# Kernel optimization log

Hardware: AMD Instinct MI355X
Metric: run time of the kernel (lower is better)

The kernel has to match this reference:

```python
import jax, jax.numpy as jnp
import numpy as np

EPS = 1e-12  # torch F.normalize eps

def _l2norm(v, axis):
    n = jnp.sqrt(jnp.sum(v * v, axis=axis, keepdims=True))
    return v / jnp.maximum(n, EPS)

def setup_inputs() -> dict:
    key = jax.random.key(0)
    k1, k2, k3 = jax.random.split(key, 3)
    N, C, H, W, K = 64, 512, 32, 32, 64
    x = jax.random.normal(k1, (N, C, H, W), dtype=jnp.float32)
    conv_w = jax.random.normal(k2, (K, C), dtype=jnp.float32) * 0.05
    centroids = jax.random.uniform(k3, (K, C), dtype=jnp.float32)
    return {"x": x, "conv_w": conv_w, "centroids": centroids}

def reference(x, conv_w, centroids):
    N, C, H, W = x.shape
    K = centroids.shape[0]
    # descriptor-wise L2 normalization over channel dim
    x = _l2norm(x, axis=1)
    xf = x.reshape(N, C, H * W)                       # (N, C, S)
    # 1x1 conv (no bias) == per-pixel matmul, then softmax over clusters
    logits = jnp.einsum('kc,ncs->nks', conv_w, xf)    # (N, K, S)
    a = jax.nn.softmax(logits, axis=1)                # softmax over clusters
    # vlad[n,k,:] = sum_s a[n,k,s] * (x[n,:,s] - centroid[k])
    # = (a @ x^T) - centroid * sum_s a   -- two GEMM-like ops, no (N,K,C,S) tensor
    vlad = jnp.einsum('nks,ncs->nkc', a, xf) - a.sum(axis=-1)[..., None] * centroids[None, :, :]
    # intra-normalization per cluster, flatten, global L2 norm
    vlad = _l2norm(vlad, axis=2)
    vlad = vlad.reshape(N, K * C)
    vlad = _l2norm(vlad, axis=1)
    return vlad
```

## Files before the change

kernel.cpp:

```cpp
#include <hip/hip_runtime.h>
#include <hip/hip_bf16.h>
#include <math.h>

#define EPSF 1e-12f

typedef __attribute__((ext_vector_type(8))) short bf16x8;
typedef __attribute__((ext_vector_type(4))) float f32x4;
typedef __attribute__((ext_vector_type(4))) short short4v;
typedef __attribute__((ext_vector_type(4))) unsigned short ushort4v;

static __device__ __forceinline__ short f2bf(float f) {
  union { __hip_bfloat16 h; short s; } u;
  u.h = __float2bfloat16(f);
  return u.s;
}

__global__ __launch_bounds__(256) void k2_mfma(
    const float* __restrict__ x, const float* __restrict__ w,
    unsigned short* __restrict__ ap, float* __restrict__ suma) {
  __shared__ __align__(16) float xf[64][70];
  __shared__ __align__(16) short wb[64][72];
  __shared__ __align__(16) float red[4][64];
  __shared__ float invs[64];
  __shared__ float gmaxs[64];
  __shared__ float gsums[64];

  const int n = blockIdx.y;
  const int s0 = blockIdx.x << 6;
  const int t = threadIdx.x;
  const int lane = t & 63;
  const int wid = t >> 6;
  const int col = t & 15;
  const int quad = (t >> 4) & 3;
  const int cr = t >> 4;
  const int sg = t & 15;

  f32x4 acc[4] = {{0,0,0,0},{0,0,0,0},{0,0,0,0},{0,0,0,0}};
  float ssq0 = 0.f, ssq1 = 0.f, ssq2 = 0.f, ssq3 = 0.f;

  for (int c0 = 0; c0 < 512; c0 += 64) {
#pragma unroll
    for (int p = 0; p < 4; ++p) {
      int c = cr + (p << 4);
      float4 g = *(const float4*)&x[((size_t)((n << 9) + c0 + c) << 10) + s0 + (sg << 2)];
      float2 glo; glo.x = g.x; glo.y = g.y;
      float2 ghi; ghi.x = g.z; ghi.y = g.w;
      *(float2*)&xf[c][sg << 2] = glo;
      *(float2*)&xf[c][(sg << 2) + 2] = ghi;
      ssq0 = fmaf(g.x, g.x, ssq0); ssq1 = fmaf(g.y, g.y, ssq1);
      ssq2 = fmaf(g.z, g.z, ssq2); ssq3 = fmaf(g.w, g.w, ssq3);
      float4 gw = *(const float4*)&w[(c << 9) + c0 + (sg << 2)];
      short4v hw; hw.x = f2bf(gw.x); hw.y = f2bf(gw.y); hw.z = f2bf(gw.z); hw.w = f2bf(gw.w);
      *(short4v*)&wb[c][sg << 2] = hw;
    }
    __syncthreads();
#pragma unroll
    for (int cc = 0; cc < 64; cc += 32) {
      bf16x8 af = *(const bf16x8*)&wb[(wid << 4) + col][cc + (quad << 3)];
      int cb = cc + (quad << 3);
#pragma unroll
      for (int sgr = 0; sgr < 4; ++sgr) {
        int sc = (sgr << 4) + col;
        bf16x8 bfr;
#pragma unroll
        for (int j = 0; j < 8; ++j) bfr[j] = f2bf(xf[cb + j][sc]);
        acc[sgr] = __builtin_amdgcn_mfma_f32_16x16x32_bf16(af, bfr, acc[sgr], 0, 0, 0);
      }
    }
    __syncthreads();
  }

  ssq0 += __shfl_xor(ssq0, 16, 64); ssq0 += __shfl_xor(ssq0, 32, 64);
  ssq1 += __shfl_xor(ssq1, 16, 64); ssq1 += __shfl_xor(ssq1, 32, 64);
  ssq2 += __shfl_xor(ssq2, 16, 64); ssq2 += __shfl_xor(ssq2, 32, 64);
  ssq3 += __shfl_xor(ssq3, 16, 64); ssq3 += __shfl_xor(ssq3, 32, 64);
  if (lane < 16) {
    float4 v; v.x = ssq0; v.y = ssq1; v.z = ssq2; v.w = ssq3;
    *(float4*)&red[wid][sg << 2] = v;
  }
  __syncthreads();
  if (t < 64) {
    float tot = red[0][t] + red[1][t] + red[2][t] + red[3][t];
    invs[t] = 1.0f / fmaxf(sqrtf(tot), EPSF);
  }
  __syncthreads();

  float li[4];
#pragma unroll
  for (int sgr = 0; sgr < 4; ++sgr) li[sgr] = invs[(sgr << 4) + col];
  float le[4][4];
#pragma unroll
  for (int sgr = 0; sgr < 4; ++sgr)
#pragma unroll
    for (int r = 0; r < 4; ++r) le[sgr][r] = acc[sgr][r] * li[sgr];

  float mx[4];
#pragma unroll
  for (int sgr = 0; sgr < 4; ++sgr) {
    float m = fmaxf(fmaxf(le[sgr][0], le[sgr][1]), fmaxf(le[sgr][2], le[sgr][3]));
    m = fmaxf(m, __shfl_xor(m, 16, 64));
    m = fmaxf(m, __shfl_xor(m, 32, 64));
    mx[sgr] = m;
  }
  if (lane < 16) {
#pragma unroll
    for (int sgr = 0; sgr < 4; ++sgr) red[wid][(sgr << 4) + sg] = mx[sgr];
  }
  __syncthreads();
  if (t < 64)
    gmaxs[t] = fmaxf(fmaxf(red[0][t], red[1][t]), fmaxf(red[2][t], red[3][t]));
  __syncthreads();

  float ps[4];
#pragma unroll
  for (int sgr = 0; sgr < 4; ++sgr) {
    float gm = gmaxs[(sgr << 4) + col];
    float p = 0.f;
#pragma unroll
    for (int r = 0; r < 4; ++r) {
      float e = __expf(le[sgr][r] - gm);
      le[sgr][r] = e;
      p += e;
    }
    p += __shfl_xor(p, 16, 64);
    p += __shfl_xor(p, 32, 64);
    ps[sgr] = p;
  }
  if (lane < 16) {
#pragma unroll
    for (int sgr = 0; sgr < 4; ++sgr) red[wid][(sgr << 4) + sg] = ps[sgr];
  }
  __syncthreads();
  if (t < 64) gsums[t] = red[0][t] + red[1][t] + red[2][t] + red[3][t];
  __syncthreads();

  float sk[4] = {0.f, 0.f, 0.f, 0.f};
#pragma unroll
  for (int sgr = 0; sgr < 4; ++sgr) {
    float rinv = 1.0f / gsums[(sgr << 4) + col];
#pragma unroll
    for (int r = 0; r < 4; ++r) {
      float av = le[sgr][r] * rinv;
      sk[r] += av;
      float apv = av * li[sgr];
      int k = (wid << 4) + (quad << 2) + r;
      ap[((size_t)((n << 6) + k) << 10) + s0 + (sgr << 4) + col] =
          (unsigned short)f2bf(apv);
    }
  }
#pragma unroll
  for (int r = 0; r < 4; ++r) {
    sk[r] += __shfl_xor(sk[r], 1, 64);
    sk[r] += __shfl_xor(sk[r], 2, 64);
    sk[r] += __shfl_xor(sk[r], 4, 64);
    sk[r] += __shfl_xor(sk[r], 8, 64);
  }
  if (col == 0) {
#pragma unroll
    for (int r = 0; r < 4; ++r)
      atomicAdd(&suma[(n << 6) + (wid << 4) + (quad << 2) + r], sk[r]);
  }
}

__global__ __launch_bounds__(256) void k3_mfma(
    const float* __restrict__ x, const unsigned short* __restrict__ ap,
    const float* __restrict__ cent, const float* __restrict__ suma,
    float* __restrict__ out, float* __restrict__ rnorm2) {
  __shared__ __align__(16) char sm[64 * 72 * 2 * 2];
  short (*xb)[72] = reinterpret_cast<short(*)[72]>(sm);
  short (*at)[72] = reinterpret_cast<short(*)[72]>(sm + 9216);
  float (*lt)[68] = reinterpret_cast<float(*)[68]>(sm);

  const int n = blockIdx.y;
  const int c0 = blockIdx.x << 6;
  const int t = threadIdx.x;
  const int lane = t & 63;
  const int wid = t >> 6;
  const int col = t & 15;
  const int quad = (t >> 4) & 3;
  const int cr = t >> 4;
  const int sg = t & 15;

  f32x4 acc[4] = {{0,0,0,0},{0,0,0,0},{0,0,0,0},{0,0,0,0}};

  for (int s0 = 0; s0 < 1024; s0 += 64) {
#pragma unroll
    for (int p = 0; p < 4; ++p) {
      int c = cr + (p << 4);
      float4 g = *(const float4*)&x[((size_t)((n << 9) + c0 + c) << 10) + s0 + (sg << 2)];
      short4v hx; hx.x = f2bf(g.x); hx.y = f2bf(g.y); hx.z = f2bf(g.z); hx.w = f2bf(g.w);
      *(short4v*)&xb[c][sg << 2] = hx;
      ushort4v a4 = *(const ushort4v*)&ap[((size_t)((n << 6) + c) << 10) + s0 + (sg << 2)];
      *(ushort4v*)&at[c][sg << 2] = a4;
    }
    __syncthreads();
#pragma unroll
    for (int ss = 0; ss < 64; ss += 32) {
      bf16x8 af = *(const bf16x8*)&xb[(wid << 4) + col][ss + (quad << 3)];
#pragma unroll
      for (int kt = 0; kt < 4; ++kt) {
        bf16x8 bfr = *(const bf16x8*)&at[(kt << 4) + col][ss + (quad << 3)];
        acc[kt] = __builtin_amdgcn_mfma_f32_16x16x32_bf16(af, bfr, acc[kt], 0, 0, 0);
      }
    }
    __syncthreads();
  }

  float sa[4];
#pragma unroll
  for (int kt = 0; kt < 4; ++kt) sa[kt] = suma[(n << 6) + (kt << 4) + col];
  const int crow = (wid << 4) + (quad << 2);
  float r2[4] = {0.f, 0.f, 0.f, 0.f};
#pragma unroll
  for (int kt = 0; kt < 4; ++kt) {
    int k = (kt << 4) + col;
#pragma unroll
    for (int r = 0; r < 4; ++r) {
      int c = crow + r;
      float ce = cent[(k << 9) + c0 + c];
      float val = acc[kt][r] - sa[kt] * ce;
      r2[kt] = fmaf(val, val, r2[kt]);
      lt[k][c] = val;
    }
  }
#pragma unroll
  for (int kt = 0; kt < 4; ++kt) {
    r2[kt] += __shfl_xor(r2[kt], 16, 64);
    r2[kt] += __shfl_xor(r2[kt], 32, 64);
  }
  if (lane < 16) {
#pragma unroll
    for (int kt = 0; kt < 4; ++kt)
      atomicAdd(&rnorm2[(n << 6) + (kt << 4) + sg], r2[kt]);
  }
  __syncthreads();
#pragma unroll
  for (int u = 0; u < 4; ++u) {
    int k = t >> 2;
    int c = ((t & 3) << 2) + (u << 4);
    float4 v = *(const float4*)&lt[k][c];
    *(float4*)&out[((size_t)((n << 6) + k) << 9) + c0 + c] = v;
  }
}

__global__ __launch_bounds__(64) void k4_factors(const float* __restrict__ rnorm2,
                                                 float* __restrict__ fac) {
  int n = blockIdx.x, k = threadIdx.x;
  float r2 = rnorm2[(n << 6) + k];
  float rn = sqrtf(r2);
  float f = 1.0f / fmaxf(rn, EPSF);
  float nr = rn * f;
  float g = nr * nr;
#pragma unroll
  for (int off = 32; off > 0; off >>= 1) g += __shfl_xor(g, off, 64);
  fac[(n << 6) + k] = f * (1.0f / fmaxf(sqrtf(g), EPSF));
}

__global__ __launch_bounds__(256) void k5_scale(const float* __restrict__ vlad,
                                                const float* __restrict__ fac,
                                                float* __restrict__ out) {
  int idx = blockIdx.x * 256 + threadIdx.x;
  float4 v = ((const float4*)vlad)[idx];
  float f = fac[idx >> 7];
  float4 o;
  o.x = v.x * f; o.y = v.y * f; o.z = v.z * f; o.w = v.w * f;
  ((float4*)out)[idx] = o;
}

extern "C" void kernel_launch(void* const* d_in, const int* in_sizes, int n_in,
                              void* d_out, int out_size, void* d_ws, size_t ws_size,
                              hipStream_t stream) {
  (void)in_sizes; (void)n_in; (void)out_size; (void)ws_size;
  const float* x = (const float*)d_in[0];
  const float* w = (const float*)d_in[1];
  const float* cent = (const float*)d_in[2];
  float* out = (float*)d_out;

  float* ws = (float*)d_ws;
  float* suma = ws;
  float* rnorm2 = ws + 4096;
  float* fac = ws + 8192;
  unsigned short* ap = (unsigned short*)(ws + 12288);

  hipMemsetAsync(ws, 0, 8192 * sizeof(float), stream);
  k2_mfma<<<dim3(16, 64), 256, 0, stream>>>(x, w, ap, suma);
  k3_mfma<<<dim3(8, 64), 256, 0, stream>>>(x, ap, cent, suma, out, rnorm2);
  k4_factors<<<64, 64, 0, stream>>>(rnorm2, fac);
  k5_scale<<<2048, 256, 0, stream>>>(out, fac, out);
}
```

Baseline: 259.0 us.

## Register-prefetch k3 tiles, swap grid order, fold factor kernel into scale

k3 now double-buffers its global loads in registers, issuing the next tile's x and assignment loads before the MFMAs on the current tile, so memory latency overlaps compute. The grid is transposed so consecutive blocks take different batch items instead of channel slices of the same item. The separate k4 factor kernel is removed: each k5 block recomputes the per-cluster and global norm factors from rnorm2, saving one launch at the cost of redundant sqrt work and extra register pressure.

```diff
diff --git a/kernel.cpp b/kernel.cpp
--- a/kernel.cpp
+++ b/kernel.cpp
@@ -162,6 +162,37 @@
   }
 }
 
+#define K3_LOADT(gx, ga, S0)                                                   \
+  do {                                                                         \
+    _Pragma("unroll") for (int p = 0; p < 4; ++p) {                            \
+      gx[p] = *(const float4*)(xbase + ((size_t)(p << 4) << 10) + (S0));       \
+      ga[p] = *(const ushort4v*)(abase + ((size_t)(p << 4) << 10) + (S0));     \
+    }                                                                          \
+  } while (0)
+
+#define K3_WRITET(gx, ga)                                                      \
+  do {                                                                         \
+    _Pragma("unroll") for (int p = 0; p < 4; ++p) {                            \
+      int c = cr + (p << 4);                                                   \
+      short4v hx;                                                              \
+      hx.x = f2bf(gx[p].x); hx.y = f2bf(gx[p].y);                              \
+      hx.z = f2bf(gx[p].z); hx.w = f2bf(gx[p].w);                              \
+      *(short4v*)&xb[c][sg << 2] = hx;                                         \
+      *(ushort4v*)&at[c][sg << 2] = ga[p];                                     \
+    }                                                                          \
+  } while (0)
+
+#define K3_MFMAT()                                                             \
+  do {                                                                         \
+    _Pragma("unroll") for (int ss = 0; ss < 64; ss += 32) {                    \
+      bf16x8 af = *(const bf16x8*)&xb[(wid << 4) + col][ss + (quad << 3)];     \
+      _Pragma("unroll") for (int kt = 0; kt < 4; ++kt) {                       \
+        bf16x8 bfr = *(const bf16x8*)&at[(kt << 4) + col][ss + (quad << 3)];   \
+        acc[kt] = __builtin_amdgcn_mfma_f32_16x16x32_bf16(af, bfr, acc[kt], 0, 0, 0); \
+      }                                                                        \
+    }                                                                          \
+  } while (0)
+
 __global__ __launch_bounds__(256) void k3_mfma(
     const float* __restrict__ x, const unsigned short* __restrict__ ap,
     const float* __restrict__ cent, const float* __restrict__ suma,
@@ -171,8 +202,8 @@
   short (*at)[72] = reinterpret_cast<short(*)[72]>(sm + 9216);
   float (*lt)[68] = reinterpret_cast<float(*)[68]>(sm);
 
-  const int n = blockIdx.y;
-  const int c0 = blockIdx.x << 6;
+  const int n = blockIdx.x;
+  const int c0 = blockIdx.y << 6;
   const int t = threadIdx.x;
   const int lane = t & 63;
   const int wid = t >> 6;
@@ -183,26 +214,26 @@
 
   f32x4 acc[4] = {{0,0,0,0},{0,0,0,0},{0,0,0,0},{0,0,0,0}};
 
-  for (int s0 = 0; s0 < 1024; s0 += 64) {
-#pragma unroll
-    for (int p = 0; p < 4; ++p) {
-      int c = cr + (p << 4);
-      float4 g = *(const float4*)&x[((size_t)((n << 9) + c0 + c) << 10) + s0 + (sg << 2)];
-      short4v hx; hx.x = f2bf(g.x); hx.y = f2bf(g.y); hx.z = f2bf(g.z); hx.w = f2bf(g.w);
-      *(short4v*)&xb[c][sg << 2] = hx;
-      ushort4v a4 = *(const ushort4v*)&ap[((size_t)((n << 6) + c) << 10) + s0 + (sg << 2)];
-      *(ushort4v*)&at[c][sg << 2] = a4;
-    }
-    __syncthreads();
-#pragma unroll
-    for (int ss = 0; ss < 64; ss += 32) {
-      bf16x8 af = *(const bf16x8*)&xb[(wid << 4) + col][ss + (quad << 3)];
-#pragma unroll
-      for (int kt = 0; kt < 4; ++kt) {
-        bf16x8 bfr = *(const bf16x8*)&at[(kt << 4) + col][ss + (quad << 3)];
-        acc[kt] = __builtin_amdgcn_mfma_f32_16x16x32_bf16(af, bfr, acc[kt], 0, 0, 0);
-      }
-    }
+  const float* xbase = &x[((size_t)((n << 9) + c0 + cr) << 10) + (sg << 2)];
+  const unsigned short* abase = &ap[((size_t)((n << 6) + cr) << 10) + (sg << 2)];
+
+  float4 gxA[4]; ushort4v gaA[4];
+  float4 gxB[4]; ushort4v gaB[4];
+
+  K3_LOADT(gxA, gaA, 0);
+#pragma unroll 1
+  for (int it = 0; it < 8; ++it) {
+    K3_WRITET(gxA, gaA);
+    __syncthreads();
+    K3_LOADT(gxB, gaB, (size_t)(((it << 1) + 1) << 6));
+    K3_MFMAT();
+    __syncthreads();
+    K3_WRITET(gxB, gaB);
+    __syncthreads();
+    if (it < 7) {
+      K3_LOADT(gxA, gaA, (size_t)(((it << 1) + 2) << 6));
+    }
+    K3_MFMAT();
     __syncthreads();
   }
 
@@ -243,25 +274,28 @@
   }
 }
 
-__global__ __launch_bounds__(64) void k4_factors(const float* __restrict__ rnorm2,
-                                                 float* __restrict__ fac) {
-  int n = blockIdx.x, k = threadIdx.x;
-  float r2 = rnorm2[(n << 6) + k];
-  float rn = sqrtf(r2);
-  float f = 1.0f / fmaxf(rn, EPSF);
-  float nr = rn * f;
-  float g = nr * nr;
-#pragma unroll
-  for (int off = 32; off > 0; off >>= 1) g += __shfl_xor(g, off, 64);
-  fac[(n << 6) + k] = f * (1.0f / fmaxf(sqrtf(g), EPSF));
-}
-
 __global__ __launch_bounds__(256) void k5_scale(const float* __restrict__ vlad,
-                                                const float* __restrict__ fac,
+                                                const float* __restrict__ rnorm2,
                                                 float* __restrict__ out) {
-  int idx = blockIdx.x * 256 + threadIdx.x;
+  __shared__ float gsh;
+  const int b = blockIdx.x;
+  const int t = threadIdx.x;
+  const int n = b >> 5;
+  if (t < 64) {
+    float rn = sqrtf(rnorm2[(n << 6) + t]);
+    float nr = rn / fmaxf(rn, EPSF);
+    float g = nr * nr;
+#pragma unroll
+    for (int off = 32; off > 0; off >>= 1) g += __shfl_xor(g, off, 64);
+    if (t == 0) gsh = g;
+  }
+  __syncthreads();
+  const float ginv = 1.0f / fmaxf(sqrtf(gsh), EPSF);
+  const int idx = (b << 8) + t;
+  const int kg = idx >> 7;
+  float rn = sqrtf(rnorm2[kg]);
+  float f = (1.0f / fmaxf(rn, EPSF)) * ginv;
   float4 v = ((const float4*)vlad)[idx];
-  float f = fac[idx >> 7];
   float4 o;
   o.x = v.x * f; o.y = v.y * f; o.z = v.z * f; o.w = v.w * f;
   ((float4*)out)[idx] = o;
@@ -279,12 +313,10 @@
   float* ws = (float*)d_ws;
   float* suma = ws;
   float* rnorm2 = ws + 4096;
-  float* fac = ws + 8192;
   unsigned short* ap = (unsigned short*)(ws + 12288);
 
   hipMemsetAsync(ws, 0, 8192 * sizeof(float), stream);
   k2_mfma<<<dim3(16, 64), 256, 0, stream>>>(x, w, ap, suma);
-  k3_mfma<<<dim3(8, 64), 256, 0, stream>>>(x, ap, cent, suma, out, rnorm2);
-  k4_factors<<<64, 64, 0, stream>>>(rnorm2, fac);
-  k5_scale<<<2048, 256, 0, stream>>>(out, fac, out);
-}
+  k3_mfma<<<dim3(64, 8), 256, 0, stream>>>(x, ap, cent, suma, out, rnorm2);
+  k5_scale<<<2048, 256, 0, stream>>>(out, rnorm2, out);
+}
```

New measurement: 229.4 us. -11.4%, faster.
